# Kernel optimization log

Measured on AMD Instinct MI355X. Metric: run time of the kernel, lower is better.

## Reference

```python
import jax, jax.numpy as jnp
import numpy as np

HIDDEN = 1024
FFN = 2048
NUM_EXPERTS = 8
TOP_K = 2
BATCH, SEQ = 2, 1024


def setup_inputs() -> dict:
    key = jax.random.key(0)
    k0, k1, k2, k3, k4 = jax.random.split(key, 5)
    scale = 0.02
    hidden_states = jax.random.normal(k0, (BATCH, SEQ, HIDDEN), dtype=jnp.float32)
    gate_w = jax.random.normal(k1, (NUM_EXPERTS, HIDDEN), dtype=jnp.float32) * scale
    w1 = jax.random.normal(k2, (NUM_EXPERTS, FFN, HIDDEN), dtype=jnp.float32) * scale  # gate proj
    w3 = jax.random.normal(k3, (NUM_EXPERTS, FFN, HIDDEN), dtype=jnp.float32) * scale  # up proj
    w2 = jax.random.normal(k4, (NUM_EXPERTS, HIDDEN, FFN), dtype=jnp.float32) * scale  # down proj
    return {"hidden_states": hidden_states, "gate_w": gate_w, "w1": w1, "w2": w2, "w3": w3}


def reference(hidden_states, gate_w, w1, w2, w3):
    B, S, D = hidden_states.shape
    x = hidden_states.reshape(-1, D)                         # [T, D]
    T = x.shape[0]
    # Router: logits -> fp32 softmax -> top-k -> renormalize
    router_logits = jnp.einsum("td,ed->te", x, gate_w)       # [T, E]
    routing_weights = jax.nn.softmax(router_logits.astype(jnp.float32), axis=1)
    top_vals, top_idx = jax.lax.top_k(routing_weights, TOP_K)  # [T, K]
    top_vals = top_vals / jnp.sum(top_vals, axis=-1, keepdims=True)
    top_vals = top_vals.astype(x.dtype)
    # Per-token-per-expert combine weight (0 for unselected experts)
    w_te = jnp.zeros((T, NUM_EXPERTS), dtype=x.dtype)
    w_te = w_te.at[jnp.arange(T)[:, None], top_idx].add(top_vals)  # [T, E]
    # Fused experts: silu(x W1^T) * (x W3^T) -> W2^T, weighted combine
    g = jax.nn.silu(jnp.einsum("td,efd->tef", x, w1))        # [T, E, F]
    u = jnp.einsum("td,efd->tef", x, w3)                     # [T, E, F]
    y = jnp.einsum("tef,edf->ted", g * u, w2)                # [T, E, D]
    out = jnp.einsum("ted,te->td", y, w_te)                  # [T, D]
    return out.reshape(B, S, D), router_logits
```

## Files before the change

kernel.cpp:

```cpp
#include <hip/hip_runtime.h>
#include <hip/hip_bf16.h>
#include <stdint.h>

#define HIDDEN  1024
#define FFN_DIM 2048
#define NEXP    8
#define NTOK    2048
#define MAXROWS 5120

typedef short bf16x8 __attribute__((ext_vector_type(8)));
typedef float f32x4  __attribute__((ext_vector_type(4)));

static const size_t OFF_CNT  = 0;
static const size_t OFF_BASE = 64;
static const size_t OFF_TOK  = 128;
static const size_t OFF_WGT  = OFF_TOK + (size_t)NEXP*NTOK*4;
static const size_t OFF_XBF  = 131328;
static const size_t XBF_B    = (size_t)NTOK*HIDDEN*2;
static const size_t OFF_H    = OFF_XBF + XBF_B;
static const size_t H_B      = (size_t)MAXROWS*FFN_DIM*2;
static const size_t WS_NEED  = OFF_H + H_B;

__device__ __forceinline__ unsigned short f2bf(float f) {
  union { float f; unsigned u; } a; a.f = f;
  unsigned r = a.u + 0x7fff + ((a.u >> 16) & 1);
  return (unsigned short)(r >> 16);
}

__device__ __forceinline__ uint4 cvt8(float4 a, float4 b) {
  uint4 r;
  asm("v_cvt_pk_bf16_f32 %0, %1, %2" : "=v"(r.x) : "v"(a.x), "v"(a.y));
  asm("v_cvt_pk_bf16_f32 %0, %1, %2" : "=v"(r.y) : "v"(a.z), "v"(a.w));
  asm("v_cvt_pk_bf16_f32 %0, %1, %2" : "=v"(r.z) : "v"(b.x), "v"(b.y));
  asm("v_cvt_pk_bf16_f32 %0, %1, %2" : "=v"(r.w) : "v"(b.z), "v"(b.w));
  return r;
}

__device__ __forceinline__ void ld_g2l16(const void* gsrc, void* ldst) {
  __builtin_amdgcn_global_load_lds(
      (const __attribute__((address_space(1))) unsigned int*)gsrc,
      (__attribute__((address_space(3))) unsigned int*)ldst, 16, 0, 0);
}

__global__ __launch_bounds__(256) void router_kernel(
    const float* __restrict__ x, const float* __restrict__ gw,
    float* __restrict__ logits, int* __restrict__ cnt,
    int* __restrict__ tok, float* __restrict__ wgt)
{
  const int t   = blockIdx.x;
  const int tid = threadIdx.x;
  float4 xv = ((const float4*)(x + (size_t)t * HIDDEN))[tid];
  float p[NEXP];
#pragma unroll
  for (int e = 0; e < NEXP; ++e) {
    float4 gv = ((const float4*)(gw + (size_t)e * HIDDEN))[tid];
    p[e] = xv.x * gv.x + xv.y * gv.y + xv.z * gv.z + xv.w * gv.w;
  }
#pragma unroll
  for (int e = 0; e < NEXP; ++e) {
#pragma unroll
    for (int off = 32; off > 0; off >>= 1)
      p[e] += __shfl_down(p[e], off, 64);
  }
  __shared__ float red[4][NEXP];
  const int wv = tid >> 6, ln = tid & 63;
  if (ln == 0) {
#pragma unroll
    for (int e = 0; e < NEXP; ++e) red[wv][e] = p[e];
  }
  __syncthreads();
  if (tid == 0) {
    float l[NEXP];
#pragma unroll
    for (int e = 0; e < NEXP; ++e) {
      l[e] = red[0][e] + red[1][e] + red[2][e] + red[3][e];
      logits[(size_t)t * NEXP + e] = l[e];
    }
    int i0 = 0;
#pragma unroll
    for (int e = 1; e < NEXP; ++e) if (l[e] > l[i0]) i0 = e;
    int i1 = (i0 == 0) ? 1 : 0;
#pragma unroll
    for (int e = 0; e < NEXP; ++e) if (e != i0 && l[e] > l[i1]) i1 = e;
    float w0 = 1.f / (1.f + expf(l[i1] - l[i0]));
    float w1 = 1.f - w0;
    int s0 = atomicAdd(&cnt[i0], 1);
    tok[i0 * NTOK + s0] = t;  wgt[i0 * NTOK + s0] = w0;
    int s1 = atomicAdd(&cnt[i1], 1);
    tok[i1 * NTOK + s1] = t;  wgt[i1 * NTOK + s1] = w1;
  }
}

__global__ void prefix_kernel(const int* __restrict__ cnt, int* __restrict__ base) {
  if (threadIdx.x == 0 && blockIdx.x == 0) {
    int b = 0;
#pragma unroll
    for (int e = 0; e < NEXP; ++e) { base[e] = b; b += ((cnt[e] + 127) >> 7) << 7; }
    base[NEXP] = b;
  }
}

__global__ __launch_bounds__(256) void cvt_kernel(
    const float* __restrict__ src, unsigned short* __restrict__ dst, int n4)
{
  int i = blockIdx.x * blockDim.x + threadIdx.x;
  const int stride = gridDim.x * blockDim.x;
  for (; i < n4; i += stride) {
    float4 v = ((const float4*)src)[i];
    ushort4 o;
    o.x = f2bf(v.x); o.y = f2bf(v.y); o.z = f2bf(v.z); o.w = f2bf(v.w);
    ((ushort4*)dst)[i] = o;
  }
}

__global__ __launch_bounds__(512, 4) void gemm1_kernel(
    const unsigned short* __restrict__ xbf,
    const float* __restrict__ w1f,
    const float* __restrict__ w3f,
    const int* __restrict__ cnt, const int* __restrict__ base,
    const int* __restrict__ tok,
    unsigned short* __restrict__ H)
{
  const int bid  = blockIdx.x;
  const int e    = bid & 7;
  const int slot = bid >> 3;
  const int mt   = slot & 15;
  const int nt   = slot >> 4;
  const int n = cnt[e];
  if (mt * 128 >= n) return;
  const int t = threadIdx.x;
  const int w = t >> 6, l = t & 63;

  __shared__ unsigned short Xs [128 * 64];
  __shared__ unsigned short W1s[128 * 64];
  __shared__ unsigned short W3s[128 * 64];
  __shared__ int stok[128];

  if (t < 128) {
    int idx = mt * 128 + t;
    stok[t] = tok[e * NTOK + min(idx, n - 1)];
  }
  __syncthreads();

  const int r0 = t >> 3;
  const size_t tok0 = (size_t)stok[r0];
  const size_t tok1 = (size_t)stok[64 + r0];
  const int kp = (((t & 7) ^ ((t >> 3) & 7)) << 3);

  const float* w1e = w1f + (size_t)e * FFN_DIM * HIDDEN + (size_t)(nt * 128) * HIDDEN;
  const float* w3e = w3f + (size_t)e * FFN_DIM * HIDDEN + (size_t)(nt * 128) * HIDDEN;
  const float* w1p0 = w1e + (size_t)r0        * HIDDEN + kp;
  const float* w1p1 = w1e + (size_t)(64 + r0) * HIDDEN + kp;
  const float* w3p0 = w3e + (size_t)r0        * HIDDEN + kp;
  const float* w3p1 = w3e + (size_t)(64 + r0) * HIDDEN + kp;

  uint4* lw1a = (uint4*)((char*)W1s + t * 16);
  uint4* lw1b = (uint4*)((char*)W1s + 8192 + t * 16);
  uint4* lw3a = (uint4*)((char*)W3s + t * 16);
  uint4* lw3b = (uint4*)((char*)W3s + 8192 + t * 16);
  char* ldsX = (char*)Xs + w * 1024;

  f32x4 acc1[4][2], acc3[4][2];
#pragma unroll
  for (int i = 0; i < 4; ++i)
#pragma unroll
    for (int j = 0; j < 2; ++j) { acc1[i][j] = (f32x4)0.f; acc3[i][j] = (f32x4)0.f; }

  const int Moff = (w & 1) * 64;
  const int Noff = (w >> 1) * 32;
  const int lr = l & 15;
  const int lg = l >> 4;

  for (int kb = 0; kb < HIDDEN / 64; ++kb) {
    __syncthreads();
    const int kofs = kb * 64 + kp;
    ld_g2l16(xbf + tok0 * HIDDEN + kofs, ldsX);
    ld_g2l16(xbf + tok1 * HIDDEN + kofs, ldsX + 8192);
    {
      const int ko = kb * 64;
      float4 a0 = *(const float4*)(w1p0 + ko);
      float4 a1 = *(const float4*)(w1p0 + ko + 4);
      float4 a2 = *(const float4*)(w1p1 + ko);
      float4 a3 = *(const float4*)(w1p1 + ko + 4);
      float4 b0 = *(const float4*)(w3p0 + ko);
      float4 b1 = *(const float4*)(w3p0 + ko + 4);
      float4 b2 = *(const float4*)(w3p1 + ko);
      float4 b3 = *(const float4*)(w3p1 + ko + 4);
      *lw1a = cvt8(a0, a1);
      *lw1b = cvt8(a2, a3);
      *lw3a = cvt8(b0, b1);
      *lw3b = cvt8(b2, b3);
    }
    __syncthreads();
#pragma unroll
    for (int s = 0; s < 2; ++s) {
      const int ug = 4 * s + lg;
      bf16x8 a[4], b1v[2], b3v[2];
#pragma unroll
      for (int mi = 0; mi < 4; ++mi) {
        const int R = Moff + mi * 16 + lr;
        a[mi] = *(const bf16x8*)&Xs[R * 64 + ((ug ^ (lr & 7)) << 3)];
      }
#pragma unroll
      for (int ni = 0; ni < 2; ++ni) {
        const int R = Noff + ni * 16 + lr;
        b1v[ni] = *(const bf16x8*)&W1s[R * 64 + ((ug ^ (lr & 7)) << 3)];
        b3v[ni] = *(const bf16x8*)&W3s[R * 64 + ((ug ^ (lr & 7)) << 3)];
      }
#pragma unroll
      for (int mi = 0; mi < 4; ++mi)
#pragma unroll
        for (int ni = 0; ni < 2; ++ni) {
          acc1[mi][ni] = __builtin_amdgcn_mfma_f32_16x16x32_bf16(a[mi], b1v[ni], acc1[mi][ni], 0, 0, 0);
          acc3[mi][ni] = __builtin_amdgcn_mfma_f32_16x16x32_bf16(a[mi], b3v[ni], acc3[mi][ni], 0, 0, 0);
        }
    }
  }

  const size_t rbase = (size_t)base[e] + (size_t)mt * 128;
#pragma unroll
  for (int mi = 0; mi < 4; ++mi)
#pragma unroll
    for (int ni = 0; ni < 2; ++ni)
#pragma unroll
      for (int j = 0; j < 4; ++j) {
        int row = Moff + mi * 16 + lg * 4 + j;
        int col = nt * 128 + Noff + ni * 16 + lr;
        float s1 = acc1[mi][ni][j], s3 = acc3[mi][ni][j];
        float h = (s1 / (1.f + __expf(-s1))) * s3;
        H[(rbase + row) * FFN_DIM + col] = f2bf(h);
      }
}

__global__ __launch_bounds__(512, 4) void gemm2_kernel(
    const unsigned short* __restrict__ H,
    const float* __restrict__ w2f,
    const int* __restrict__ cnt, const int* __restrict__ base,
    const int* __restrict__ tok, const float* __restrict__ wgt,
    float* __restrict__ out)
{
  const int bid  = blockIdx.x;
  const int e    = bid & 7;
  const int slot = bid >> 3;
  const int mt   = slot & 15;
  const int nt   = slot >> 4;
  const int n = cnt[e];
  if (mt * 128 >= n) return;
  const int t = threadIdx.x;
  const int w = t >> 6, l = t & 63;

  __shared__ unsigned short Hs[128 * 64];
  __shared__ unsigned short Ws[128 * 64];
  __shared__ int   stok[128];
  __shared__ float swgt[128];

  if (t < 128) {
    int idx = mt * 128 + t;
    int ok = idx < n;
    stok[t] = ok ? tok[e * NTOK + idx] : -1;
    swgt[t] = ok ? wgt[e * NTOK + idx] : 0.f;
  }

  const int r0 = t >> 3;
  const int kp = (((t & 7) ^ ((t >> 3) & 7)) << 3);
  const unsigned short* He = H + (size_t)(base[e] + mt * 128) * FFN_DIM;
  const float* w2e  = w2f + (size_t)e * HIDDEN * FFN_DIM + (size_t)(nt * 128) * FFN_DIM;
  const float* w2p0 = w2e + (size_t)r0        * FFN_DIM + kp;
  const float* w2p1 = w2e + (size_t)(64 + r0) * FFN_DIM + kp;

  uint4* lwa = (uint4*)((char*)Ws + t * 16);
  uint4* lwb = (uint4*)((char*)Ws + 8192 + t * 16);
  char* ldsH = (char*)Hs + w * 1024;

  f32x4 acc[4][2];
#pragma unroll
  for (int i = 0; i < 4; ++i)
#pragma unroll
    for (int j = 0; j < 2; ++j) acc[i][j] = (f32x4)0.f;

  const int Moff = (w & 1) * 64;
  const int Noff = (w >> 1) * 32;
  const int lr = l & 15;
  const int lg = l >> 4;

  for (int kb = 0; kb < FFN_DIM / 64; ++kb) {
    __syncthreads();
    const int kofs = kb * 64 + kp;
    ld_g2l16(He + (size_t)r0 * FFN_DIM + kofs,        ldsH);
    ld_g2l16(He + (size_t)(64 + r0) * FFN_DIM + kofs, ldsH + 8192);
    {
      const int ko = kb * 64;
      float4 a0 = *(const float4*)(w2p0 + ko);
      float4 a1 = *(const float4*)(w2p0 + ko + 4);
      float4 a2 = *(const float4*)(w2p1 + ko);
      float4 a3 = *(const float4*)(w2p1 + ko + 4);
      *lwa = cvt8(a0, a1);
      *lwb = cvt8(a2, a3);
    }
    __syncthreads();
#pragma unroll
    for (int s = 0; s < 2; ++s) {
      const int ug = 4 * s + lg;
      bf16x8 a[4], b[2];
#pragma unroll
      for (int mi = 0; mi < 4; ++mi) {
        const int R = Moff + mi * 16 + lr;
        a[mi] = *(const bf16x8*)&Hs[R * 64 + ((ug ^ (lr & 7)) << 3)];
      }
#pragma unroll
      for (int ni = 0; ni < 2; ++ni) {
        const int R = Noff + ni * 16 + lr;
        b[ni] = *(const bf16x8*)&Ws[R * 64 + ((ug ^ (lr & 7)) << 3)];
      }
#pragma unroll
      for (int mi = 0; mi < 4; ++mi)
#pragma unroll
        for (int ni = 0; ni < 2; ++ni)
          acc[mi][ni] = __builtin_amdgcn_mfma_f32_16x16x32_bf16(a[mi], b[ni], acc[mi][ni], 0, 0, 0);
    }
  }

#pragma unroll
  for (int mi = 0; mi < 4; ++mi)
#pragma unroll
    for (int ni = 0; ni < 2; ++ni)
#pragma unroll
      for (int j = 0; j < 4; ++j) {
        int row = Moff + mi * 16 + lg * 4 + j;
        int tk = stok[row];
        if (tk >= 0) {
          int col = nt * 128 + Noff + ni * 16 + lr;
          atomicAdd(&out[(size_t)tk * HIDDEN + col], swgt[row] * acc[mi][ni][j]);
        }
      }
}

#define TT 12
#define FC 256
#define NCHUNK (FFN_DIM / FC)

__global__ __launch_bounds__(256) void moe_ffn_kernel(
    const float* __restrict__ x,
    const float* __restrict__ w1, const float* __restrict__ w2,
    const float* __restrict__ w3,
    const int* __restrict__ cnt, const int* __restrict__ tok,
    const float* __restrict__ wgt, float* __restrict__ out)
{
  const int e  = blockIdx.y;
  const int n  = cnt[e];
  const int ts = blockIdx.x * TT;
  if (ts >= n) return;
  const int tid = threadIdx.x;

  __shared__ float xs[TT * HIDDEN];
  __shared__ float hc[TT * FC];
  __shared__ int   stok[TT];
  __shared__ float swgt[TT];

  if (tid < TT) {
    int idx = ts + tid;
    int tk  = (idx < n) ? tok[e * NTOK + idx] : -1;
    stok[tid] = tk;
    swgt[tid] = (idx < n) ? wgt[e * NTOK + idx] : 0.f;
  }
  __syncthreads();
#pragma unroll
  for (int i = 0; i < TT; ++i) {
    int tk = stok[i];
    float4 v = make_float4(0.f, 0.f, 0.f, 0.f);
    if (tk >= 0) v = ((const float4*)(x + (size_t)tk * HIDDEN))[tid];
    ((float4*)(xs + i * HIDDEN))[tid] = v;
  }
  __syncthreads();

  const float* w1e = w1 + (size_t)e * FFN_DIM * HIDDEN;
  const float* w3e = w3 + (size_t)e * FFN_DIM * HIDDEN;
  const float* w2e = w2 + (size_t)e * HIDDEN * FFN_DIM;

  float yacc[4][TT];
#pragma unroll
  for (int j = 0; j < 4; ++j)
#pragma unroll
    for (int t = 0; t < TT; ++t) yacc[j][t] = 0.f;

  for (int c = 0; c < NCHUNK; ++c) {
    const int f = c * FC + tid;
    const float4* r1 = (const float4*)(w1e + (size_t)f * HIDDEN);
    const float4* r3 = (const float4*)(w3e + (size_t)f * HIDDEN);
    float a1[TT], a3[TT];
#pragma unroll
    for (int t = 0; t < TT; ++t) { a1[t] = 0.f; a3[t] = 0.f; }
    for (int k = 0; k < HIDDEN / 4; ++k) {
      float4 v1 = r1[k];
      float4 v3 = r3[k];
#pragma unroll
      for (int t = 0; t < TT; ++t) {
        float4 xv = *(const float4*)(xs + t * HIDDEN + 4 * k);
        a1[t] += xv.x * v1.x + xv.y * v1.y + xv.z * v1.z + xv.w * v1.w;
        a3[t] += xv.x * v3.x + xv.y * v3.y + xv.z * v3.z + xv.w * v3.w;
      }
    }
    __syncthreads();
#pragma unroll
    for (int t = 0; t < TT; ++t) {
      float g  = a1[t];
      float sg = g / (1.f + __expf(-g));
      hc[t * FC + tid] = sg * a3[t];
    }
    __syncthreads();
    const float4* r20 = (const float4*)(w2e + (size_t)(tid      ) * FFN_DIM + c * FC);
    const float4* r21 = (const float4*)(w2e + (size_t)(tid + 256) * FFN_DIM + c * FC);
    const float4* r22 = (const float4*)(w2e + (size_t)(tid + 512) * FFN_DIM + c * FC);
    const float4* r23 = (const float4*)(w2e + (size_t)(tid + 768) * FFN_DIM + c * FC);
    for (int k = 0; k < FC / 4; ++k) {
      float4 wv0 = r20[k], wv1 = r21[k], wv2 = r22[k], wv3 = r23[k];
#pragma unroll
      for (int t = 0; t < TT; ++t) {
        float4 hv = *(const float4*)(hc + t * FC + 4 * k);
        yacc[0][t] += hv.x * wv0.x + hv.y * wv0.y + hv.z * wv0.z + hv.w * wv0.w;
        yacc[1][t] += hv.x * wv1.x + hv.y * wv1.y + hv.z * wv1.z + hv.w * wv1.w;
        yacc[2][t] += hv.x * wv2.x + hv.y * wv2.y + hv.z * wv2.z + hv.w * wv2.w;
        yacc[3][t] += hv.x * wv3.x + hv.y * wv3.y + hv.z * wv3.z + hv.w * wv3.w;
      }
    }
  }

#pragma unroll
  for (int t = 0; t < TT; ++t) {
    int tk = stok[t];
    if (tk < 0) continue;
    float wt = swgt[t];
    float* orow = out + (size_t)tk * HIDDEN;
    atomicAdd(orow + tid,       wt * yacc[0][t]);
    atomicAdd(orow + tid + 256, wt * yacc[1][t]);
    atomicAdd(orow + tid + 512, wt * yacc[2][t]);
    atomicAdd(orow + tid + 768, wt * yacc[3][t]);
  }
}

extern "C" void kernel_launch(void* const* d_in, const int* in_sizes, int n_in,
                              void* d_out, int out_size, void* d_ws, size_t ws_size,
                              hipStream_t stream) {
  const float* x  = (const float*)d_in[0];
  const float* gw = (const float*)d_in[1];
  const float* w1 = (const float*)d_in[2];
  const float* w2 = (const float*)d_in[3];
  const float* w3 = (const float*)d_in[4];
  float* out    = (float*)d_out;
  float* logits = out + (size_t)NTOK * HIDDEN;

  char* ws = (char*)d_ws;
  int*   cnt  = (int*)(ws + OFF_CNT);
  int*   base = (int*)(ws + OFF_BASE);
  int*   tokp = (int*)(ws + OFF_TOK);
  float* wgtp = (float*)(ws + OFF_WGT);

  hipMemsetAsync(out, 0, (size_t)NTOK * HIDDEN * sizeof(float), stream);
  hipMemsetAsync(cnt, 0, NEXP * sizeof(int), stream);

  router_kernel<<<NTOK, 256, 0, stream>>>(x, gw, logits, cnt, tokp, wgtp);

  if (ws_size >= WS_NEED) {
    unsigned short* xbf  = (unsigned short*)(ws + OFF_XBF);
    unsigned short* Hbuf = (unsigned short*)(ws + OFF_H);

    cvt_kernel<<<512, 256, 0, stream>>>(x, xbf, (int)(NTOK * HIDDEN / 4));
    prefix_kernel<<<1, 64, 0, stream>>>(cnt, base);

    gemm1_kernel<<<NEXP * 16 * 16, 512, 0, stream>>>(xbf, w1, w3, cnt, base, tokp, Hbuf);
    gemm2_kernel<<<NEXP * 16 * 8, 512, 0, stream>>>(Hbuf, w2, cnt, base, tokp, wgtp, out);
  } else {
    dim3 grid((NTOK + TT - 1) / TT, NEXP);
    moe_ffn_kernel<<<grid, 256, 0, stream>>>(x, w1, w2, w3, cnt, tokp, wgtp, out);
  }
}
```

Before: 227.1 us.

## Halve M tile to 64 rows and split-K the down-projection GEMM

Reduces the per-block token tile from 128 to 64 rows in both expert GEMMs, pads expert segments to 64, and adds a 2-way split-K over the FFN dimension in gemm2, combined with the existing atomicAdd output. The aim is less padding waste on unevenly routed experts and more active blocks to fill the GPU. In exchange, each fp32 weight tile is re-read and re-converted to bf16 by twice as many M-blocks, roughly doubling weight traffic and conversion work, and gemm2 issues twice as many atomics.

```diff
diff --git a/kernel.cpp b/kernel.cpp
--- a/kernel.cpp
+++ b/kernel.cpp
@@ -95,7 +95,7 @@
   if (threadIdx.x == 0 && blockIdx.x == 0) {
     int b = 0;
 #pragma unroll
-    for (int e = 0; e < NEXP; ++e) { base[e] = b; b += ((cnt[e] + 127) >> 7) << 7; }
+    for (int e = 0; e < NEXP; ++e) { base[e] = b; b += ((cnt[e] + 63) >> 6) << 6; }
     base[NEXP] = b;
   }
 }
@@ -124,35 +124,27 @@
   const int bid  = blockIdx.x;
   const int e    = bid & 7;
   const int slot = bid >> 3;
-  const int mt   = slot & 15;
-  const int nt   = slot >> 4;
+  const int mt   = slot & 31;
+  const int nt   = slot >> 5;
   const int n = cnt[e];
-  if (mt * 128 >= n) return;
+  if (mt * 64 >= n) return;
   const int t = threadIdx.x;
   const int w = t >> 6, l = t & 63;
 
-  __shared__ unsigned short Xs [128 * 64];
+  __shared__ unsigned short Xs [64 * 64];
   __shared__ unsigned short W1s[128 * 64];
   __shared__ unsigned short W3s[128 * 64];
-  __shared__ int stok[128];
-
-  if (t < 128) {
-    int idx = mt * 128 + t;
-    stok[t] = tok[e * NTOK + min(idx, n - 1)];
-  }
-  __syncthreads();
-
-  const int r0 = t >> 3;
-  const size_t tok0 = (size_t)stok[r0];
-  const size_t tok1 = (size_t)stok[64 + r0];
+
+  const int rX = t >> 3;
+  const size_t tok0 = (size_t)tok[e * NTOK + min(mt * 64 + rX, n - 1)];
   const int kp = (((t & 7) ^ ((t >> 3) & 7)) << 3);
 
   const float* w1e = w1f + (size_t)e * FFN_DIM * HIDDEN + (size_t)(nt * 128) * HIDDEN;
   const float* w3e = w3f + (size_t)e * FFN_DIM * HIDDEN + (size_t)(nt * 128) * HIDDEN;
-  const float* w1p0 = w1e + (size_t)r0        * HIDDEN + kp;
-  const float* w1p1 = w1e + (size_t)(64 + r0) * HIDDEN + kp;
-  const float* w3p0 = w3e + (size_t)r0        * HIDDEN + kp;
-  const float* w3p1 = w3e + (size_t)(64 + r0) * HIDDEN + kp;
+  const float* w1p0 = w1e + (size_t)rX        * HIDDEN + kp;
+  const float* w1p1 = w1e + (size_t)(64 + rX) * HIDDEN + kp;
+  const float* w3p0 = w3e + (size_t)rX        * HIDDEN + kp;
+  const float* w3p1 = w3e + (size_t)(64 + rX) * HIDDEN + kp;
 
   uint4* lw1a = (uint4*)((char*)W1s + t * 16);
   uint4* lw1b = (uint4*)((char*)W1s + 8192 + t * 16);
@@ -160,22 +152,20 @@
   uint4* lw3b = (uint4*)((char*)W3s + 8192 + t * 16);
   char* ldsX = (char*)Xs + w * 1024;
 
-  f32x4 acc1[4][2], acc3[4][2];
-#pragma unroll
-  for (int i = 0; i < 4; ++i)
+  f32x4 acc1[2][2], acc3[2][2];
+#pragma unroll
+  for (int i = 0; i < 2; ++i)
 #pragma unroll
     for (int j = 0; j < 2; ++j) { acc1[i][j] = (f32x4)0.f; acc3[i][j] = (f32x4)0.f; }
 
-  const int Moff = (w & 1) * 64;
+  const int Moff = (w & 1) * 32;
   const int Noff = (w >> 1) * 32;
   const int lr = l & 15;
   const int lg = l >> 4;
 
   for (int kb = 0; kb < HIDDEN / 64; ++kb) {
     __syncthreads();
-    const int kofs = kb * 64 + kp;
-    ld_g2l16(xbf + tok0 * HIDDEN + kofs, ldsX);
-    ld_g2l16(xbf + tok1 * HIDDEN + kofs, ldsX + 8192);
+    ld_g2l16(xbf + tok0 * HIDDEN + kb * 64 + kp, ldsX);
     {
       const int ko = kb * 64;
       float4 a0 = *(const float4*)(w1p0 + ko);
@@ -195,9 +185,9 @@
 #pragma unroll
     for (int s = 0; s < 2; ++s) {
       const int ug = 4 * s + lg;
-      bf16x8 a[4], b1v[2], b3v[2];
-#pragma unroll
-      for (int mi = 0; mi < 4; ++mi) {
+      bf16x8 a[2], b1v[2], b3v[2];
+#pragma unroll
+      for (int mi = 0; mi < 2; ++mi) {
         const int R = Moff + mi * 16 + lr;
         a[mi] = *(const bf16x8*)&Xs[R * 64 + ((ug ^ (lr & 7)) << 3)];
       }
@@ -208,7 +198,7 @@
         b3v[ni] = *(const bf16x8*)&W3s[R * 64 + ((ug ^ (lr & 7)) << 3)];
       }
 #pragma unroll
-      for (int mi = 0; mi < 4; ++mi)
+      for (int mi = 0; mi < 2; ++mi)
 #pragma unroll
         for (int ni = 0; ni < 2; ++ni) {
           acc1[mi][ni] = __builtin_amdgcn_mfma_f32_16x16x32_bf16(a[mi], b1v[ni], acc1[mi][ni], 0, 0, 0);
@@ -217,9 +207,9 @@
     }
   }
 
-  const size_t rbase = (size_t)base[e] + (size_t)mt * 128;
-#pragma unroll
-  for (int mi = 0; mi < 4; ++mi)
+  const size_t rbase = (size_t)base[e] + (size_t)mt * 64;
+#pragma unroll
+  for (int mi = 0; mi < 2; ++mi)
 #pragma unroll
     for (int ni = 0; ni < 2; ++ni)
 #pragma unroll
@@ -242,54 +232,54 @@
   const int bid  = blockIdx.x;
   const int e    = bid & 7;
   const int slot = bid >> 3;
-  const int mt   = slot & 15;
-  const int nt   = slot >> 4;
+  const int mt   = slot & 31;
+  const int nt   = (slot >> 5) & 7;
+  const int sk   = slot >> 8;
   const int n = cnt[e];
-  if (mt * 128 >= n) return;
+  if (mt * 64 >= n) return;
   const int t = threadIdx.x;
   const int w = t >> 6, l = t & 63;
 
-  __shared__ unsigned short Hs[128 * 64];
+  __shared__ unsigned short Hs[64 * 64];
   __shared__ unsigned short Ws[128 * 64];
-  __shared__ int   stok[128];
-  __shared__ float swgt[128];
-
-  if (t < 128) {
-    int idx = mt * 128 + t;
+  __shared__ int   stok[64];
+  __shared__ float swgt[64];
+
+  if (t < 64) {
+    int idx = mt * 64 + t;
     int ok = idx < n;
     stok[t] = ok ? tok[e * NTOK + idx] : -1;
     swgt[t] = ok ? wgt[e * NTOK + idx] : 0.f;
   }
 
-  const int r0 = t >> 3;
+  const int rH = t >> 3;
   const int kp = (((t & 7) ^ ((t >> 3) & 7)) << 3);
-  const unsigned short* He = H + (size_t)(base[e] + mt * 128) * FFN_DIM;
+  const unsigned short* He = H + (size_t)(base[e] + mt * 64) * FFN_DIM;
   const float* w2e  = w2f + (size_t)e * HIDDEN * FFN_DIM + (size_t)(nt * 128) * FFN_DIM;
-  const float* w2p0 = w2e + (size_t)r0        * FFN_DIM + kp;
-  const float* w2p1 = w2e + (size_t)(64 + r0) * FFN_DIM + kp;
+  const float* w2p0 = w2e + (size_t)rH        * FFN_DIM + kp;
+  const float* w2p1 = w2e + (size_t)(64 + rH) * FFN_DIM + kp;
 
   uint4* lwa = (uint4*)((char*)Ws + t * 16);
   uint4* lwb = (uint4*)((char*)Ws + 8192 + t * 16);
   char* ldsH = (char*)Hs + w * 1024;
 
-  f32x4 acc[4][2];
-#pragma unroll
-  for (int i = 0; i < 4; ++i)
+  f32x4 acc[2][2];
+#pragma unroll
+  for (int i = 0; i < 2; ++i)
 #pragma unroll
     for (int j = 0; j < 2; ++j) acc[i][j] = (f32x4)0.f;
 
-  const int Moff = (w & 1) * 64;
+  const int Moff = (w & 1) * 32;
   const int Noff = (w >> 1) * 32;
   const int lr = l & 15;
   const int lg = l >> 4;
-
-  for (int kb = 0; kb < FFN_DIM / 64; ++kb) {
-    __syncthreads();
-    const int kofs = kb * 64 + kp;
-    ld_g2l16(He + (size_t)r0 * FFN_DIM + kofs,        ldsH);
-    ld_g2l16(He + (size_t)(64 + r0) * FFN_DIM + kofs, ldsH + 8192);
+  const int kbase = sk * (FFN_DIM / 2);
+
+  for (int kb = 0; kb < FFN_DIM / 2 / 64; ++kb) {
+    __syncthreads();
+    const int ko = kbase + kb * 64;
+    ld_g2l16(He + (size_t)rH * FFN_DIM + ko + kp, ldsH);
     {
-      const int ko = kb * 64;
       float4 a0 = *(const float4*)(w2p0 + ko);
       float4 a1 = *(const float4*)(w2p0 + ko + 4);
       float4 a2 = *(const float4*)(w2p1 + ko);
@@ -301,9 +291,9 @@
 #pragma unroll
     for (int s = 0; s < 2; ++s) {
       const int ug = 4 * s + lg;
-      bf16x8 a[4], b[2];
-#pragma unroll
-      for (int mi = 0; mi < 4; ++mi) {
+      bf16x8 a[2], b[2];
+#pragma unroll
+      for (int mi = 0; mi < 2; ++mi) {
         const int R = Moff + mi * 16 + lr;
         a[mi] = *(const bf16x8*)&Hs[R * 64 + ((ug ^ (lr & 7)) << 3)];
       }
@@ -313,7 +303,7 @@
         b[ni] = *(const bf16x8*)&Ws[R * 64 + ((ug ^ (lr & 7)) << 3)];
       }
 #pragma unroll
-      for (int mi = 0; mi < 4; ++mi)
+      for (int mi = 0; mi < 2; ++mi)
 #pragma unroll
         for (int ni = 0; ni < 2; ++ni)
           acc[mi][ni] = __builtin_amdgcn_mfma_f32_16x16x32_bf16(a[mi], b[ni], acc[mi][ni], 0, 0, 0);
@@ -321,7 +311,7 @@
   }
 
 #pragma unroll
-  for (int mi = 0; mi < 4; ++mi)
+  for (int mi = 0; mi < 2; ++mi)
 #pragma unroll
     for (int ni = 0; ni < 2; ++ni)
 #pragma unroll
@@ -467,8 +457,8 @@
     cvt_kernel<<<512, 256, 0, stream>>>(x, xbf, (int)(NTOK * HIDDEN / 4));
     prefix_kernel<<<1, 64, 0, stream>>>(cnt, base);
 
-    gemm1_kernel<<<NEXP * 16 * 16, 512, 0, stream>>>(xbf, w1, w3, cnt, base, tokp, Hbuf);
-    gemm2_kernel<<<NEXP * 16 * 8, 512, 0, stream>>>(Hbuf, w2, cnt, base, tokp, wgtp, out);
+    gemm1_kernel<<<NEXP * 32 * 16, 512, 0, stream>>>(xbf, w1, w3, cnt, base, tokp, Hbuf);
+    gemm2_kernel<<<NEXP * 32 * 8 * 2, 512, 0, stream>>>(Hbuf, w2, cnt, base, tokp, wgtp, out);
   } else {
     dim3 grid((NTOK + TT - 1) / TT, NEXP);
     moe_ffn_kernel<<<grid, 256, 0, stream>>>(x, w1, w2, w3, cnt, tokp, wgtp, out);
```

New measurement: 217.5 us. 1.04x faster.
